# Kernel tuning notes

Measured on AMD Instinct MI355X. Metric: run time of the kernel, lower is better.

The kernel has to match this reference:

```python
import jax, jax.numpy as jnp
import numpy as np
from jax.scipy.special import logsumexp

V, E, H, T, L = 50000, 256, 128, 64, 4096
D = int(np.log2(L))          # leaves live at heap level D
N = 2 * L - 1                # total nodes in perfect binary tree (heap indexing)


def _postorder(n_total):
    order = []
    def rec(i):
        if 2 * i + 1 < n_total:
            rec(2 * i + 1)
            rec(2 * i + 2)
        order.append(i)
    rec(0)
    return np.array(order, dtype=np.int32)

POST = _postorder(N)


def setup_inputs() -> dict:
    key = jax.random.key(0)
    ks = jax.random.split(key, 8)
    s = lambda k, shape, fan: (jax.random.normal(k, shape, jnp.float32) / np.sqrt(fan).astype(np.float32))
    return {
        "tokens": jax.random.randint(ks[0], (L,), 0, V),
        "emb": s(ks[1], (V, E), E),
        "W_ih": s(ks[2], (4 * H, E), E),
        "W_hh": s(ks[3], (4 * H, H), H),
        "b_ih": jnp.zeros((4 * H,), jnp.float32),
        "b_hh": jnp.zeros((4 * H,), jnp.float32),
        "W_p2h": s(ks[4], (H, 2 * H), 2 * H),
        "b_p2h": jnp.zeros((H,), jnp.float32),
        "W_uni": s(ks[5], (T, H), H),
        "b_uni": jnp.zeros((T,), jnp.float32),
        "W_edge": s(ks[6], (T * T, 2 * H), 2 * H),
        "b_edge": jnp.zeros((T * T,), jnp.float32),
    }


def reference(tokens, emb, W_ih, W_hh, b_ih, b_hh, W_p2h, b_p2h,
              W_uni, b_uni, W_edge, b_edge):
    # ---- Encoder: embedding + single-layer LSTM over the leaf sequence ----
    x = emb[tokens]                                   # [L, E]
    def step(carry, xt):
        h, c = carry
        g = W_ih @ xt + b_ih + W_hh @ h + b_hh        # torch gate order i,f,g,o
        i, f, gg, o = jnp.split(g, 4)
        c = jax.nn.sigmoid(f) * c + jax.nn.sigmoid(i) * jnp.tanh(gg)
        h = jax.nn.sigmoid(o) * jnp.tanh(c)
        return (h, c), h
    z = jnp.zeros((H,), x.dtype)
    _, leaf_h = jax.lax.scan(step, (z, z), x)         # [L, H]

    # ---- build_node_to_hidden: bottom-up per-level pair fusion ----
    hidden = jnp.zeros((N, H), x.dtype).at[L - 1:].set(leaf_h)
    for d in range(D - 1, -1, -1):
        idx = jnp.arange(2 ** d - 1, 2 ** (d + 1) - 1)
        pair = jnp.concatenate([hidden[2 * idx + 1], hidden[2 * idx + 2]], axis=1)
        hidden = hidden.at[idx].set(pair @ W_p2h.T + b_p2h)

    # ---- build_factors (batched over all nodes / edges) ----
    unary = hidden @ W_uni.T + b_uni                  # [N, T]
    child = jnp.arange(1, N)
    parent = (child - 1) // 2
    pair = jnp.concatenate([hidden[parent], hidden[child]], axis=1)
    edge_fac = (pair @ W_edge.T + b_edge).reshape(N - 1, T, T)  # edge (parent,child), idx = child-1

    # ---- upward pass (level-synchronous, bottom-up) ----
    v2f = unary                                       # node -> top factor message
    f2p = jnp.zeros((N, T), x.dtype)                  # factor -> parent message, indexed by child
    for d in range(D, -1, -1):
        idx = jnp.arange(2 ** d - 1, 2 ** (d + 1) - 1)
        if d < D:  # internal nodes: add both children's factor->node messages
            v2f = v2f.at[idx].add(f2p[2 * idx + 1] + f2p[2 * idx + 2])
        if d > 0:  # message through top edge factor to the parent
            f2p = f2p.at[idx].set(
                logsumexp(edge_fac[idx - 1] + v2f[idx][:, None, :], axis=2))

    # ---- downward pass (level-synchronous, top-down) ----
    f2n = jnp.zeros((N, T), x.dtype)                  # top-factor -> node message; root gets none
    for d in range(1, D + 1):
        idx = jnp.arange(2 ** d - 1, 2 ** (d + 1) - 1)
        par = (idx - 1) // 2
        sib = jnp.where(idx % 2 == 1, idx + 1, idx - 1)
        p2f = unary[par] + f2n[par] + f2p[sib]        # parent's messages, excluding this child's
        f2n = f2n.at[idx].set(
            logsumexp(edge_fac[idx - 1] + p2f[:, :, None], axis=1))

    beliefs = v2f + f2n                               # sum of all incoming messages, [N, T]
    return beliefs[POST]                              # stacked in postorder, like the original
```

## Files before the change

kernel.cpp:

```cpp
#include <hip/hip_runtime.h>
#include <hip/hip_bf16.h>

typedef __hip_bfloat16 bf16;
typedef float fx2 __attribute__((ext_vector_type(2)));

#define NL 4096
#define NH 128
#define NE 256
#define NT 64
#define NNODE 8191
#define NDEPTH 12

#define OF_WIH   0
#define OF_WHH   131072
#define OF_BIH   196608
#define OF_BHH   197120
#define OF_WP2H  197632
#define OF_BP2H  230400
#define OF_WUNI  230528
#define OF_BUNI  238720
#define OF_WEDGE 238784
#define OF_BEDGE 1287360
#define WF_TOTAL 1291456

__device__ __forceinline__ float b2f(bf16 x) { return __bfloat162float(x); }

__global__ void detect_kernel(const void* __restrict__ wedge_raw, int* __restrict__ flag) {
  __shared__ int cnt_sh[256];
  const unsigned short* p = (const unsigned short*)wedge_raw;
  int c = 0;
  for (int i = threadIdx.x; i < 32768; i += 256) {
    float v = __uint_as_float(((unsigned)p[2 * i]) << 16);
    if (fabsf(v) > 4.f) c++;
  }
  cnt_sh[threadIdx.x] = c;
  __syncthreads();
  for (int s = 128; s > 0; s >>= 1) {
    if (threadIdx.x < s) cnt_sh[threadIdx.x] += cnt_sh[threadIdx.x + s];
    __syncthreads();
  }
  if (threadIdx.x == 0) *flag = cnt_sh[0];
}

__global__ void convert_kernel(const void* s0, const void* s1, const void* s2, const void* s3,
                               const void* s4, const void* s5, const void* s6, const void* s7,
                               const void* s8, const void* s9,
                               const int* __restrict__ flag, float* __restrict__ wf) {
  int i = blockIdx.x * 256 + threadIdx.x;
  if (i >= WF_TOTAL) return;
  const void* src; int local;
  if      (i < OF_WHH)   { src = s0; local = i; }
  else if (i < OF_BIH)   { src = s1; local = i - OF_WHH; }
  else if (i < OF_BHH)   { src = s2; local = i - OF_BIH; }
  else if (i < OF_WP2H)  { src = s3; local = i - OF_BHH; }
  else if (i < OF_BP2H)  { src = s4; local = i - OF_WP2H; }
  else if (i < OF_WUNI)  { src = s5; local = i - OF_BP2H; }
  else if (i < OF_BUNI)  { src = s6; local = i - OF_WUNI; }
  else if (i < OF_WEDGE) { src = s7; local = i - OF_BUNI; }
  else if (i < OF_BEDGE) { src = s8; local = i - OF_WEDGE; }
  else                   { src = s9; local = i - OF_BEDGE; }
  bool isf32 = (*flag) > 100;
  wf[i] = isf32 ? ((const float*)src)[local] : b2f(((const bf16*)src)[local]);
}

__global__ __launch_bounds__(512) void g1_kernel(const int* __restrict__ tokens,
                                                 const void* __restrict__ emb_raw,
                                                 const int* __restrict__ flag,
                                                 const float* __restrict__ wf,
                                                 float* __restrict__ G1) {
  __shared__ __attribute__((aligned(16))) float xs[8 * NE];
  const bool isf32 = (*flag) > 100;
  const int t0 = blockIdx.x * 8;
  for (int q = threadIdx.x; q < 8 * NE; q += 512) {
    int tok = q >> 8, e = q & 255;
    size_t off = (size_t)tokens[t0 + tok] * NE + e;
    xs[q] = isf32 ? ((const float*)emb_raw)[off] : b2f(((const bf16*)emb_raw)[off]);
  }
  __syncthreads();
  const int r = threadIdx.x;
  const float bias = wf[OF_BIH + r] + wf[OF_BHH + r];
  float acc[8];
#pragma unroll
  for (int k = 0; k < 8; ++k) acc[k] = bias;
  const float4* W4 = (const float4*)(wf + OF_WIH + (size_t)r * NE);
#pragma unroll 8
  for (int j = 0; j < 64; ++j) {
    float4 wv = W4[j];
#pragma unroll
    for (int tok = 0; tok < 8; ++tok) {
      float4 xv = ((const float4*)(xs + tok * NE))[j];
      acc[tok] += wv.x * xv.x + wv.y * xv.y + wv.z * xv.z + wv.w * xv.w;
    }
  }
#pragma unroll
  for (int tok = 0; tok < 8; ++tok) G1[(size_t)(t0 + tok) * 512 + r] = acc[tok];
}

__global__ __launch_bounds__(512) void lstm_kernel(const float* __restrict__ wf,
                                                   const float* __restrict__ G1,
                                                   float* __restrict__ hidden) {
  const int r = threadIdx.x;
  __shared__ __attribute__((aligned(16))) float h_sh[NH];
  __shared__ float g_sh[512];
  fx2 w[64];
  const float4* W4 = (const float4*)(wf + OF_WHH + (size_t)r * NH);
#pragma unroll
  for (int j = 0; j < 32; ++j) {
    float4 v = W4[j];
    fx2 p0, p1; p0.x = v.x; p0.y = v.y; p1.x = v.z; p1.y = v.w;
    w[2 * j] = p0; w[2 * j + 1] = p1;
  }
  float c = 0.f;
  if (r < NH) h_sh[r] = 0.f;
  __syncthreads();
  float gnext = G1[r];
  for (int t = 0; t < NL; ++t) {
    float gcur = gnext;
    if (t + 1 < NL) gnext = G1[(size_t)(t + 1) * 512 + r];
    fx2 a0 = {0.f, 0.f}, a1 = {0.f, 0.f}, a2 = {0.f, 0.f}, a3 = {0.f, 0.f};
    const float4* h4 = (const float4*)h_sh;
#pragma unroll
    for (int j = 0; j < 16; ++j) {
      float4 h0 = h4[2 * j], h1 = h4[2 * j + 1];
      fx2 e0, e1, e2, e3;
      e0.x = h0.x; e0.y = h0.y; e1.x = h0.z; e1.y = h0.w;
      e2.x = h1.x; e2.y = h1.y; e3.x = h1.z; e3.y = h1.w;
      a0 += w[4 * j + 0] * e0;
      a1 += w[4 * j + 1] * e1;
      a2 += w[4 * j + 2] * e2;
      a3 += w[4 * j + 3] * e3;
    }
    g_sh[r] = gcur + (a0.x + a0.y) + (a1.x + a1.y) + (a2.x + a2.y) + (a3.x + a3.y);
    __syncthreads();
    if (r < NH) {
      float iv = g_sh[r], fv = g_sh[r + 128], gv = g_sh[r + 256], ov = g_sh[r + 384];
      float si = 1.f / (1.f + __expf(-iv));
      float sf = 1.f / (1.f + __expf(-fv));
      float tg = 1.f - 2.f / (__expf(2.f * gv) + 1.f);
      float so = 1.f / (1.f + __expf(-ov));
      c = sf * c + si * tg;
      float hh = so * (1.f - 2.f / (__expf(2.f * c) + 1.f));
      h_sh[r] = hh;
      hidden[(size_t)(NL - 1 + t) * NH + r] = hh;
    }
    __syncthreads();
  }
}

__global__ void p2h_kernel(const float* __restrict__ wf, float* __restrict__ hidden, int base) {
  int node = base + blockIdx.x;
  int j = threadIdx.x;
  __shared__ __attribute__((aligned(16))) float pr[2 * NH];
  const float* hl = hidden + (size_t)(2 * node + 1) * NH;
  pr[j] = hl[j];
  pr[j + NH] = hl[j + NH];
  __syncthreads();
  float acc = wf[OF_BP2H + j];
  const float4* W4 = (const float4*)(wf + OF_WP2H + (size_t)j * 2 * NH);
  const float4* p4 = (const float4*)pr;
#pragma unroll 16
  for (int q = 0; q < 64; ++q) {
    float4 u = W4[q], x = p4[q];
    acc += u.x * x.x + u.y * x.y + u.z * x.z + u.w * x.w;
  }
  hidden[(size_t)node * NH + j] = acc;
}

__global__ void unary_kernel(const float* __restrict__ wf, const float* __restrict__ hidden,
                             float* __restrict__ unary, float* __restrict__ f2n) {
  int node = blockIdx.x;
  int ct = threadIdx.x;
  __shared__ __attribute__((aligned(16))) float hs[NH];
  hs[ct] = hidden[(size_t)node * NH + ct];
  hs[ct + 64] = hidden[(size_t)node * NH + 64 + ct];
  __syncthreads();
  float acc = wf[OF_BUNI + ct];
  const float4* W4 = (const float4*)(wf + OF_WUNI + (size_t)ct * NH);
  const float4* h4 = (const float4*)hs;
#pragma unroll
  for (int q = 0; q < 32; ++q) {
    float4 u = W4[q], x = h4[q];
    acc += u.x * x.x + u.y * x.y + u.z * x.z + u.w * x.w;
  }
  unary[(size_t)node * NT + ct] = acc;
  if (node == 0) f2n[ct] = 0.f;
}

__global__ __launch_bounds__(256) void edge_kernel(const float* __restrict__ hidden,
                                                   const float* __restrict__ wf,
                                                   float* __restrict__ edge) {
  __shared__ __attribute__((aligned(16))) float As[32][132];
  __shared__ __attribute__((aligned(16))) float Bs[32][132];
  const int tid = threadIdx.x;
  const int nb = blockIdx.x;
  const int mb = blockIdx.y;
  const int tm = tid >> 4, tn = tid & 15;
  float acc[8][8];
#pragma unroll
  for (int i = 0; i < 8; ++i)
#pragma unroll
    for (int j = 0; j < 8; ++j) acc[i][j] = 0.f;
  const int sr = tid >> 1;
  const int sq = tid & 1;
  for (int ch = 0; ch < 8; ++ch) {
    {
      int gm = mb * 128 + sr;
      const float* srcA = (ch < 4) ? hidden + (size_t)(gm >> 1) * NH + ch * 32
                                   : hidden + (size_t)(gm + 1) * NH + (ch - 4) * 32;
      bool ok = (gm < NNODE - 1);
#pragma unroll
      for (int i = 0; i < 4; ++i) {
        int kk = sq * 16 + i * 4;
        float4 v = ok ? *(const float4*)(srcA + kk) : make_float4(0.f, 0.f, 0.f, 0.f);
        As[kk + 0][sr] = v.x; As[kk + 1][sr] = v.y; As[kk + 2][sr] = v.z; As[kk + 3][sr] = v.w;
      }
    }
    {
      int gn = nb * 128 + sr;
      const float* srcB = wf + OF_WEDGE + (size_t)gn * NE + ch * 32;
#pragma unroll
      for (int i = 0; i < 4; ++i) {
        int kk = sq * 16 + i * 4;
        float4 v = *(const float4*)(srcB + kk);
        Bs[kk + 0][sr] = v.x; Bs[kk + 1][sr] = v.y; Bs[kk + 2][sr] = v.z; Bs[kk + 3][sr] = v.w;
      }
    }
    __syncthreads();
#pragma unroll 8
    for (int kk = 0; kk < 32; ++kk) {
      float a[8], b[8];
      *(float4*)(a)     = *(const float4*)&As[kk][tm * 4];
      *(float4*)(a + 4) = *(const float4*)&As[kk][64 + tm * 4];
      *(float4*)(b)     = *(const float4*)&Bs[kk][tn * 4];
      *(float4*)(b + 4) = *(const float4*)&Bs[kk][64 + tn * 4];
#pragma unroll
      for (int i = 0; i < 8; ++i)
#pragma unroll
        for (int j = 0; j < 8; ++j) acc[i][j] += a[i] * b[j];
    }
    __syncthreads();
  }
  float bias[8];
#pragma unroll
  for (int j = 0; j < 8; ++j)
    bias[j] = wf[OF_BEDGE + nb * 128 + (j >> 2) * 64 + tn * 4 + (j & 3)];
#pragma unroll
  for (int i = 0; i < 8; ++i) {
    int gm = mb * 128 + (i >> 2) * 64 + tm * 4 + (i & 3);
    if (gm < NNODE - 1) {
      float* row = edge + (size_t)gm * 4096 + nb * 128;
      float4 o0, o1;
      o0.x = acc[i][0] + bias[0]; o0.y = acc[i][1] + bias[1];
      o0.z = acc[i][2] + bias[2]; o0.w = acc[i][3] + bias[3];
      o1.x = acc[i][4] + bias[4]; o1.y = acc[i][5] + bias[5];
      o1.z = acc[i][6] + bias[6]; o1.w = acc[i][7] + bias[7];
      *(float4*)(row + tn * 4) = o0;
      *(float4*)(row + 64 + tn * 4) = o1;
    }
  }
}

__global__ void up_kernel(const float* __restrict__ unary, const float* __restrict__ edge,
                          float* __restrict__ v2f, float* __restrict__ f2p,
                          int base, int depth) {
  int node = base + blockIdx.x;
  int tid = threadIdx.x;
  __shared__ __attribute__((aligned(16))) float vs[NT];
  float vv = unary[(size_t)node * NT + tid];
  if (depth < NDEPTH)
    vv += f2p[(size_t)(2 * node + 1) * NT + tid] + f2p[(size_t)(2 * node + 2) * NT + tid];
  v2f[(size_t)node * NT + tid] = vv;
  vs[tid] = vv;
  __syncthreads();
  if (depth == 0) return;
  const float4* E4 = (const float4*)(edge + (size_t)(node - 1) * 4096 + tid * 64);
  const float4* v4 = (const float4*)vs;
  float x[NT];
#pragma unroll
  for (int q = 0; q < 16; ++q) {
    float4 e = E4[q], vq = v4[q];
    x[4 * q + 0] = e.x + vq.x; x[4 * q + 1] = e.y + vq.y;
    x[4 * q + 2] = e.z + vq.z; x[4 * q + 3] = e.w + vq.w;
  }
  float m = x[0];
#pragma unroll
  for (int i = 1; i < NT; ++i) m = fmaxf(m, x[i]);
  float s = 0.f;
#pragma unroll
  for (int i = 0; i < NT; ++i) s += __expf(x[i] - m);
  f2p[(size_t)node * NT + tid] = m + __logf(s);
}

__global__ void down_kernel(const float* __restrict__ unary, const float* __restrict__ edge,
                            const float* __restrict__ f2p, float* __restrict__ f2n,
                            int base) {
  int node = base + blockIdx.x;
  int tid = threadIdx.x;
  int par = (node - 1) >> 1;
  int sib = (node & 1) ? node + 1 : node - 1;
  __shared__ __attribute__((aligned(16))) float us[NT];
  us[tid] = unary[(size_t)par * NT + tid] + f2n[(size_t)par * NT + tid] +
            f2p[(size_t)sib * NT + tid];
  __syncthreads();
  float uu[NT];
  const float4* u4 = (const float4*)us;
#pragma unroll
  for (int q = 0; q < 16; ++q) {
    float4 t4 = u4[q];
    uu[4 * q] = t4.x; uu[4 * q + 1] = t4.y; uu[4 * q + 2] = t4.z; uu[4 * q + 3] = t4.w;
  }
  const float* E = edge + (size_t)(node - 1) * 4096 + tid;
  float x[NT];
#pragma unroll
  for (int p = 0; p < NT; ++p) x[p] = E[(size_t)p * 64] + uu[p];
  float m = x[0];
#pragma unroll
  for (int i = 1; i < NT; ++i) m = fmaxf(m, x[i]);
  float s = 0.f;
#pragma unroll
  for (int i = 0; i < NT; ++i) s += __expf(x[i] - m);
  f2n[(size_t)node * NT + tid] = m + __logf(s);
}

__global__ void final_kernel(const float* __restrict__ v2f, const float* __restrict__ f2n,
                             const int* __restrict__ flag, void* __restrict__ out) {
  int node = blockIdx.x;
  int tid = threadIdx.x;
  unsigned v = (unsigned)node + 1u;
  int d = 31 - __clz((int)v);
  int b0 = 0, S = NNODE;
  for (int b = d - 1; b >= 0; --b) {
    int sz = (S - 1) >> 1;
    if ((v >> b) & 1) b0 += sz;
    S = sz;
  }
  int pos = b0 + S - 1;
  float val = v2f[(size_t)node * NT + tid] + f2n[(size_t)node * NT + tid];
  if ((*flag) > 100) ((float*)out)[(size_t)pos * NT + tid] = val;
  else               ((bf16*)out)[(size_t)pos * NT + tid] = __float2bfloat16(val);
}

extern "C" void kernel_launch(void* const* d_in, const int* in_sizes, int n_in,
                              void* d_out, int out_size, void* d_ws, size_t ws_size,
                              hipStream_t stream) {
  (void)in_sizes; (void)n_in; (void)out_size; (void)ws_size;
  const int* tokens = (const int*)d_in[0];

  float* ws     = (float*)d_ws;
  int*   flag   = (int*)ws;
  float* wf     = ws + 16;
  float* hidden = wf + WF_TOTAL;
  float* G1     = hidden + (size_t)NNODE * NH;
  float* unary  = G1 + (size_t)NL * 512;
  float* v2f    = unary + (size_t)NNODE * NT;
  float* f2p    = v2f + (size_t)NNODE * NT;
  float* f2n    = f2p + (size_t)NNODE * NT;
  float* edge   = f2n + (size_t)NNODE * NT;

  detect_kernel<<<1, 256, 0, stream>>>(d_in[10], flag);
  convert_kernel<<<(WF_TOTAL + 255) / 256, 256, 0, stream>>>(
      d_in[2], d_in[3], d_in[4], d_in[5], d_in[6], d_in[7],
      d_in[8], d_in[9], d_in[10], d_in[11], flag, wf);
  g1_kernel<<<NL / 8, 512, 0, stream>>>(tokens, d_in[1], flag, wf, G1);
  lstm_kernel<<<1, 512, 0, stream>>>(wf, G1, hidden);
  for (int d = NDEPTH - 1; d >= 0; --d)
    p2h_kernel<<<1 << d, 128, 0, stream>>>(wf, hidden, (1 << d) - 1);
  unary_kernel<<<NNODE, 64, 0, stream>>>(wf, hidden, unary, f2n);
  edge_kernel<<<dim3(32, 64), 256, 0, stream>>>(hidden, wf, edge);
  for (int d = NDEPTH; d >= 0; --d)
    up_kernel<<<1 << d, 64, 0, stream>>>(unary, edge, v2f, f2p, (1 << d) - 1, d);
  for (int d = 1; d <= NDEPTH; ++d)
    down_kernel<<<1 << d, 64, 0, stream>>>(unary, edge, f2p, f2n, (1 << d) - 1);
  final_kernel<<<NNODE, 64, 0, stream>>>(v2f, f2n, flag, d_out);
}
```

Measured before the change: 4.117 ms.

## Restructure LSTM recurrence with split-K threads, one barrier, and fused small tree levels

The LSTM kernel now uses 256 threads. Each thread pair owns one hidden unit, computes all four gates over half of K, and combines the halves with a lane shuffle. A gate-interleaved G1 layout and a double-buffered h remove the second barrier per timestep. G1 is staged into LDS and hidden outputs are written in 32-step chunks. Separately, the top six tree levels of the upward and downward passes are merged into single-block kernels, cutting twelve launches, at the cost of running those levels on one workgroup.

Result: slower. 5.845 ms (+42.0%).

```diff
diff --git a/kernel.cpp b/kernel.cpp
--- a/kernel.cpp
+++ b/kernel.cpp
@@ -67,7 +67,7 @@
                                                  const void* __restrict__ emb_raw,
                                                  const int* __restrict__ flag,
                                                  const float* __restrict__ wf,
-                                                 float* __restrict__ G1) {
+                                                 float* __restrict__ G1T) {
   __shared__ __attribute__((aligned(16))) float xs[8 * NE];
   const bool isf32 = (*flag) > 100;
   const int t0 = blockIdx.x * 8;
@@ -92,58 +92,89 @@
       acc[tok] += wv.x * xv.x + wv.y * xv.y + wv.z * xv.z + wv.w * xv.w;
     }
   }
-#pragma unroll
-  for (int tok = 0; tok < 8; ++tok) G1[(size_t)(t0 + tok) * 512 + r] = acc[tok];
-}
-
-__global__ __launch_bounds__(512) void lstm_kernel(const float* __restrict__ wf,
-                                                   const float* __restrict__ G1,
-                                                   float* __restrict__ hidden) {
-  const int r = threadIdx.x;
-  __shared__ __attribute__((aligned(16))) float h_sh[NH];
-  __shared__ float g_sh[512];
-  fx2 w[64];
-  const float4* W4 = (const float4*)(wf + OF_WHH + (size_t)r * NH);
-#pragma unroll
-  for (int j = 0; j < 32; ++j) {
-    float4 v = W4[j];
-    fx2 p0, p1; p0.x = v.x; p0.y = v.y; p1.x = v.z; p1.y = v.w;
-    w[2 * j] = p0; w[2 * j + 1] = p1;
+  const int jj = r & 127, gg = r >> 7;
+#pragma unroll
+  for (int tok = 0; tok < 8; ++tok)
+    G1T[(size_t)(t0 + tok) * 512 + jj * 4 + gg] = acc[tok];
+}
+
+__global__ __launch_bounds__(256, 1) void lstm_kernel(const float* __restrict__ wf,
+                                                      const float* __restrict__ G1T,
+                                                      float* __restrict__ hidden) {
+  const int t = threadIdx.x;
+  const int j = t >> 1;
+  const int khalf = t & 1;
+  __shared__ __attribute__((aligned(16))) float h_sh[2][NH];
+  __shared__ __attribute__((aligned(16))) float G1buf[32 * 512];
+  __shared__ __attribute__((aligned(16))) float hstage[32 * NH];
+  fx2 w[4][32];
+#pragma unroll
+  for (int g = 0; g < 4; ++g) {
+    const float4* Wr = (const float4*)(wf + OF_WHH + (size_t)(j + 128 * g) * NH + khalf * 64);
+#pragma unroll
+    for (int q = 0; q < 16; ++q) {
+      float4 v = Wr[q];
+      fx2 a, b; a.x = v.x; a.y = v.y; b.x = v.z; b.y = v.w;
+      w[g][2 * q] = a; w[g][2 * q + 1] = b;
+    }
   }
   float c = 0.f;
-  if (r < NH) h_sh[r] = 0.f;
-  __syncthreads();
-  float gnext = G1[r];
-  for (int t = 0; t < NL; ++t) {
-    float gcur = gnext;
-    if (t + 1 < NL) gnext = G1[(size_t)(t + 1) * 512 + r];
+  if (khalf == 0) h_sh[0][j] = 0.f;
+  for (int tt = 0; tt < NL; ++tt) {
+    if ((tt & 31) == 0) {
+      if (tt > 0) {
+#pragma unroll
+        for (int i = 0; i < 4; ++i) {
+          float4 v = *(const float4*)&hstage[t * 16 + i * 4];
+          *(float4*)&hidden[(size_t)(NL - 1 + tt - 32) * NH + t * 16 + i * 4] = v;
+        }
+      }
+      const float* gsrc = G1T + (size_t)tt * 512;
+#pragma unroll
+      for (int i = 0; i < 16; ++i) {
+        float4 v = *(const float4*)&gsrc[t * 64 + i * 4];
+        *(float4*)&G1buf[t * 64 + i * 4] = v;
+      }
+      __syncthreads();
+    }
     fx2 a0 = {0.f, 0.f}, a1 = {0.f, 0.f}, a2 = {0.f, 0.f}, a3 = {0.f, 0.f};
-    const float4* h4 = (const float4*)h_sh;
-#pragma unroll
-    for (int j = 0; j < 16; ++j) {
-      float4 h0 = h4[2 * j], h1 = h4[2 * j + 1];
-      fx2 e0, e1, e2, e3;
-      e0.x = h0.x; e0.y = h0.y; e1.x = h0.z; e1.y = h0.w;
-      e2.x = h1.x; e2.y = h1.y; e3.x = h1.z; e3.y = h1.w;
-      a0 += w[4 * j + 0] * e0;
-      a1 += w[4 * j + 1] * e1;
-      a2 += w[4 * j + 2] * e2;
-      a3 += w[4 * j + 3] * e3;
-    }
-    g_sh[r] = gcur + (a0.x + a0.y) + (a1.x + a1.y) + (a2.x + a2.y) + (a3.x + a3.y);
-    __syncthreads();
-    if (r < NH) {
-      float iv = g_sh[r], fv = g_sh[r + 128], gv = g_sh[r + 256], ov = g_sh[r + 384];
-      float si = 1.f / (1.f + __expf(-iv));
-      float sf = 1.f / (1.f + __expf(-fv));
-      float tg = 1.f - 2.f / (__expf(2.f * gv) + 1.f);
-      float so = 1.f / (1.f + __expf(-ov));
-      c = sf * c + si * tg;
-      float hh = so * (1.f - 2.f / (__expf(2.f * c) + 1.f));
-      h_sh[r] = hh;
-      hidden[(size_t)(NL - 1 + t) * NH + r] = hh;
-    }
-    __syncthreads();
+    fx2 b0 = {0.f, 0.f}, b1 = {0.f, 0.f}, b2 = {0.f, 0.f}, b3 = {0.f, 0.f};
+    const float4* h4 = (const float4*)h_sh[tt & 1];
+#pragma unroll
+    for (int q = 0; q < 16; ++q) {
+      float4 hv = h4[khalf * 16 + q];
+      fx2 e0, e1; e0.x = hv.x; e0.y = hv.y; e1.x = hv.z; e1.y = hv.w;
+      a0 += w[0][2 * q] * e0; b0 += w[0][2 * q + 1] * e1;
+      a1 += w[1][2 * q] * e0; b1 += w[1][2 * q + 1] * e1;
+      a2 += w[2][2 * q] * e0; b2 += w[2][2 * q + 1] * e1;
+      a3 += w[3][2 * q] * e0; b3 += w[3][2 * q + 1] * e1;
+    }
+    float p0 = (a0.x + a0.y) + (b0.x + b0.y);
+    float p1 = (a1.x + a1.y) + (b1.x + b1.y);
+    float p2 = (a2.x + a2.y) + (b2.x + b2.y);
+    float p3 = (a3.x + a3.y) + (b3.x + b3.y);
+    p0 += __shfl_xor(p0, 1, 64);
+    p1 += __shfl_xor(p1, 1, 64);
+    p2 += __shfl_xor(p2, 1, 64);
+    p3 += __shfl_xor(p3, 1, 64);
+    float4 gq = *(const float4*)&G1buf[(tt & 31) * 512 + j * 4];
+    float iv = p0 + gq.x, fv = p1 + gq.y, gv = p2 + gq.z, ov = p3 + gq.w;
+    float si = 1.f / (1.f + __expf(-iv));
+    float sf = 1.f / (1.f + __expf(-fv));
+    float tg = 1.f - 2.f / (__expf(2.f * gv) + 1.f);
+    float so = 1.f / (1.f + __expf(-ov));
+    c = sf * c + si * tg;
+    float hh = so * (1.f - 2.f / (__expf(2.f * c) + 1.f));
+    if (khalf == 0) {
+      h_sh[(tt + 1) & 1][j] = hh;
+      hstage[(tt & 31) * NH + j] = hh;
+    }
+    __syncthreads();
+  }
+#pragma unroll
+  for (int i = 0; i < 4; ++i) {
+    float4 v = *(const float4*)&hstage[t * 16 + i * 4];
+    *(float4*)&hidden[(size_t)(NL - 1 + NL - 32) * NH + t * 16 + i * 4] = v;
   }
 }
 
@@ -272,7 +303,6 @@
   v2f[(size_t)node * NT + tid] = vv;
   vs[tid] = vv;
   __syncthreads();
-  if (depth == 0) return;
   const float4* E4 = (const float4*)(edge + (size_t)(node - 1) * 4096 + tid * 64);
   const float4* v4 = (const float4*)vs;
   float x[NT];
@@ -289,6 +319,43 @@
 #pragma unroll
   for (int i = 0; i < NT; ++i) s += __expf(x[i] - m);
   f2p[(size_t)node * NT + tid] = m + __logf(s);
+}
+
+__global__ __launch_bounds__(512) void up_small_kernel(const float* __restrict__ unary,
+                                                       const float* __restrict__ edge,
+                                                       float* __restrict__ v2f,
+                                                       float* __restrict__ f2p) {
+  const int g = threadIdx.x >> 6;
+  const int l = threadIdx.x & 63;
+  __shared__ __attribute__((aligned(16))) float vs[8][NT];
+  for (int d = 5; d >= 0; --d) {
+    const int base = (1 << d) - 1, cnt = 1 << d;
+    for (int nn = g; nn < cnt; nn += 8) {
+      int node = base + nn;
+      float vv = unary[(size_t)node * NT + l] +
+                 f2p[(size_t)(2 * node + 1) * NT + l] + f2p[(size_t)(2 * node + 2) * NT + l];
+      v2f[(size_t)node * NT + l] = vv;
+      vs[g][l] = vv;
+      if (d == 0) break;
+      const float4* E4 = (const float4*)(edge + (size_t)(node - 1) * 4096 + l * 64);
+      const float4* v4 = (const float4*)vs[g];
+      float x[NT];
+#pragma unroll
+      for (int q = 0; q < 16; ++q) {
+        float4 e = E4[q], vq = v4[q];
+        x[4 * q + 0] = e.x + vq.x; x[4 * q + 1] = e.y + vq.y;
+        x[4 * q + 2] = e.z + vq.z; x[4 * q + 3] = e.w + vq.w;
+      }
+      float m = x[0];
+#pragma unroll
+      for (int i = 1; i < NT; ++i) m = fmaxf(m, x[i]);
+      float s = 0.f;
+#pragma unroll
+      for (int i = 0; i < NT; ++i) s += __expf(x[i] - m);
+      f2p[(size_t)node * NT + l] = m + __logf(s);
+    }
+    __syncthreads();
+  }
 }
 
 __global__ void down_kernel(const float* __restrict__ unary, const float* __restrict__ edge,
@@ -320,6 +387,44 @@
 #pragma unroll
   for (int i = 0; i < NT; ++i) s += __expf(x[i] - m);
   f2n[(size_t)node * NT + tid] = m + __logf(s);
+}
+
+__global__ __launch_bounds__(512) void down_small_kernel(const float* __restrict__ unary,
+                                                         const float* __restrict__ edge,
+                                                         const float* __restrict__ f2p,
+                                                         float* __restrict__ f2n) {
+  const int g = threadIdx.x >> 6;
+  const int l = threadIdx.x & 63;
+  __shared__ __attribute__((aligned(16))) float us[8][NT];
+  for (int d = 1; d <= 5; ++d) {
+    const int base = (1 << d) - 1, cnt = 1 << d;
+    for (int nn = g; nn < cnt; nn += 8) {
+      int node = base + nn;
+      int par = (node - 1) >> 1;
+      int sib = (node & 1) ? node + 1 : node - 1;
+      us[g][l] = unary[(size_t)par * NT + l] + f2n[(size_t)par * NT + l] +
+                 f2p[(size_t)sib * NT + l];
+      float uu[NT];
+      const float4* u4 = (const float4*)us[g];
+#pragma unroll
+      for (int q = 0; q < 16; ++q) {
+        float4 t4 = u4[q];
+        uu[4 * q] = t4.x; uu[4 * q + 1] = t4.y; uu[4 * q + 2] = t4.z; uu[4 * q + 3] = t4.w;
+      }
+      const float* E = edge + (size_t)(node - 1) * 4096 + l;
+      float x[NT];
+#pragma unroll
+      for (int p = 0; p < NT; ++p) x[p] = E[(size_t)p * 64] + uu[p];
+      float m = x[0];
+#pragma unroll
+      for (int i = 1; i < NT; ++i) m = fmaxf(m, x[i]);
+      float s = 0.f;
+#pragma unroll
+      for (int i = 0; i < NT; ++i) s += __expf(x[i] - m);
+      f2n[(size_t)node * NT + l] = m + __logf(s);
+    }
+    __syncthreads();
+  }
 }
 
 __global__ void final_kernel(const float* __restrict__ v2f, const float* __restrict__ f2n,
@@ -350,8 +455,8 @@
   int*   flag   = (int*)ws;
   float* wf     = ws + 16;
   float* hidden = wf + WF_TOTAL;
-  float* G1     = hidden + (size_t)NNODE * NH;
-  float* unary  = G1 + (size_t)NL * 512;
+  float* G1T    = hidden + (size_t)NNODE * NH;
+  float* unary  = G1T + (size_t)NL * 512;
   float* v2f    = unary + (size_t)NNODE * NT;
   float* f2p    = v2f + (size_t)NNODE * NT;
   float* f2n    = f2p + (size_t)NNODE * NT;
@@ -361,15 +466,17 @@
   convert_kernel<<<(WF_TOTAL + 255) / 256, 256, 0, stream>>>(
       d_in[2], d_in[3], d_in[4], d_in[5], d_in[6], d_in[7],
       d_in[8], d_in[9], d_in[10], d_in[11], flag, wf);
-  g1_kernel<<<NL / 8, 512, 0, stream>>>(tokens, d_in[1], flag, wf, G1);
-  lstm_kernel<<<1, 512, 0, stream>>>(wf, G1, hidden);
+  g1_kernel<<<NL / 8, 512, 0, stream>>>(tokens, d_in[1], flag, wf, G1T);
+  lstm_kernel<<<1, 256, 0, stream>>>(wf, G1T, hidden);
   for (int d = NDEPTH - 1; d >= 0; --d)
     p2h_kernel<<<1 << d, 128, 0, stream>>>(wf, hidden, (1 << d) - 1);
   unary_kernel<<<NNODE, 64, 0, stream>>>(wf, hidden, unary, f2n);
   edge_kernel<<<dim3(32, 64), 256, 0, stream>>>(hidden, wf, edge);
-  for (int d = NDEPTH; d >= 0; --d)
+  for (int d = NDEPTH; d >= 6; --d)
     up_kernel<<<1 << d, 64, 0, stream>>>(unary, edge, v2f, f2p, (1 << d) - 1, d);
-  for (int d = 1; d <= NDEPTH; ++d)
+  up_small_kernel<<<1, 512, 0, stream>>>(unary, edge, v2f, f2p);
+  down_small_kernel<<<1, 512, 0, stream>>>(unary, edge, f2p, f2n);
+  for (int d = 6; d <= NDEPTH; ++d)
     down_kernel<<<1 << d, 64, 0, stream>>>(unary, edge, f2p, f2n, (1 << d) - 1);
   final_kernel<<<NNODE, 64, 0, stream>>>(v2f, f2n, flag, d_out);
 }
```
